# Kernel optimization log

Measured on AMD Instinct MI355X. Metric: run time of the kernel, lower is better.

## Reference

```python
import jax, jax.numpy as jnp
import numpy as np

N_EMBD = 1024
COND = 1024
N_HEAD = 16
B, N, NTOK = 4, 2048, 2048


def setup_inputs() -> dict:
    key = jax.random.key(0)
    ks = jax.random.split(key, 10)
    s = 0.02
    return {
        "x": jax.random.normal(ks[0], (B, N, N_EMBD), jnp.float32),
        "encoder_output": jax.random.normal(ks[1], (B, NTOK, COND), jnp.float32),
        "Wq": jax.random.normal(ks[2], (N_EMBD, N_EMBD), jnp.float32) * s,
        "bq": jnp.zeros((N_EMBD,), jnp.float32),
        "Wk": jax.random.normal(ks[3], (N_EMBD, COND), jnp.float32) * s,
        "bk": jnp.zeros((N_EMBD,), jnp.float32),
        "Wv": jax.random.normal(ks[4], (N_EMBD, COND), jnp.float32) * s,
        "bv": jnp.zeros((N_EMBD,), jnp.float32),
        "Wp": jax.random.normal(ks[5], (N_EMBD, N_EMBD), jnp.float32) * s,
        "bp": jnp.zeros((N_EMBD,), jnp.float32),
    }


def reference(x, encoder_output, Wq, bq, Wk, bk, Wv, bv, Wp, bp):
    Bx, Nx, C = x.shape
    H = N_HEAD
    D = C // H
    # projections (torch Linear: y = x @ W^T + b)
    q = (x @ Wq.T + bq).reshape(Bx, Nx, H, D)               # b n h d
    k = (encoder_output @ Wk.T + bk).reshape(Bx, -1, H, D)  # b t h d
    v = (encoder_output @ Wv.T + bv).reshape(Bx, -1, H, D)
    scale = 1.0 / jnp.sqrt(jnp.asarray(D, x.dtype))
    att = jnp.einsum("bnhd,bthd->bhnt", q, k) * scale
    att = jax.nn.softmax(att, axis=-1)
    y = jnp.einsum("bhnt,bthd->bnhd", att, v).reshape(Bx, Nx, C)
    y = y @ Wp.T + bp  # dropout is identity at inference (p effectively 0)
    return y
```

## Files before the change

kernel.cpp:

```cpp
#include <hip/hip_runtime.h>

typedef short bf16x8 __attribute__((ext_vector_type(8)));
typedef float f32x4 __attribute__((ext_vector_type(4)));
typedef unsigned int u32x2 __attribute__((ext_vector_type(2)));
typedef unsigned int u32x4 __attribute__((ext_vector_type(4)));

#define AS1 __attribute__((address_space(1)))
#define AS3 __attribute__((address_space(3)))

__device__ __forceinline__ void gld16(void* lds, const void* g) {
  __builtin_amdgcn_global_load_lds((const AS1 unsigned int*)g,
                                   (AS3 unsigned int*)lds, 16, 0, 0);
}

__device__ __forceinline__ unsigned short f2bf(float f) {
  union { float f; unsigned int u; } c; c.f = f;
  return (unsigned short)((c.u + 0x7FFFu + ((c.u >> 16) & 1u)) >> 16);
}

__device__ __forceinline__ unsigned short cvt1(float x) {
  unsigned int r;
  asm("v_cvt_pk_bf16_f32 %0, %1, %1" : "=v"(r) : "v"(x));
  return (unsigned short)r;
}

__device__ __forceinline__ unsigned int cvtpk(float lo, float hi) {
  unsigned int r;
  asm("v_cvt_pk_bf16_f32 %0, %1, %2" : "=v"(r) : "v"(lo), "v"(hi));
  return r;
}

__device__ __forceinline__ float bf2f(unsigned short u) {
  union { unsigned int u; float f; } c; c.u = ((unsigned int)u) << 16;
  return c.f;
}

__device__ __forceinline__ float fmax3(float a, float b, float c) {
  return fmaxf(fmaxf(a, b), c);
}

__global__ void cvt_kernel(const float4* __restrict__ in0,
                           const float4* __restrict__ in1,
                           ushort4* __restrict__ out0,
                           ushort4* __restrict__ out1, int n4) {
  const float4* in = blockIdx.y ? in1 : in0;
  ushort4* out = blockIdx.y ? out1 : out0;
  int i = blockIdx.x * blockDim.x + threadIdx.x;
  int stride = gridDim.x * blockDim.x;
  for (; i < n4; i += stride) {
    float4 v = in[i];
    ushort4 o;
    o.x = f2bf(v.x); o.y = f2bf(v.y); o.z = f2bf(v.z); o.w = f2bf(v.w);
    out[i] = o;
  }
}

__global__ void cvtw_kernel(const float4* w0, const float4* w1,
                            const float4* w2, const float4* w3,
                            ushort4* o0, ushort4* o1, ushort4* o2, ushort4* o3,
                            int n4) {
  const float4* in; ushort4* out;
  switch (blockIdx.y) {
    case 0: in = w0; out = o0; break;
    case 1: in = w1; out = o1; break;
    case 2: in = w2; out = o2; break;
    default: in = w3; out = o3; break;
  }
  int i = blockIdx.x * blockDim.x + threadIdx.x;
  int stride = gridDim.x * blockDim.x;
  for (; i < n4; i += stride) {
    float4 v = in[i];
    ushort4 o;
    o.x = f2bf(v.x); o.y = f2bf(v.y); o.z = f2bf(v.z); o.w = f2bf(v.w);
    out[i] = o;
  }
}

__global__ __launch_bounds__(256) void gemm_qkv_kernel(
    const unsigned short* __restrict__ Xb,
    const unsigned short* __restrict__ Eb,
    const unsigned short* __restrict__ Wqb,
    const unsigned short* __restrict__ Wkb,
    const unsigned short* __restrict__ Wvb,
    const float* __restrict__ bq,
    const float* __restrict__ bk,
    const float* __restrict__ bv,
    unsigned short* __restrict__ Qw,
    unsigned short* __restrict__ Kw,
    unsigned short* __restrict__ VTw,
    float qscale)
{
  __shared__ alignas(16) unsigned short As[2][4 * 128 * 8];
  __shared__ alignas(16) unsigned short Bs[2][4 * 128 * 8];

  const int bid = blockIdx.x;
  const int o = (bid & 7) * 192 + (bid >> 3);
  const int xx = o % 24;
  const int yy = o / 24;
  const int sec = xx >> 3;
  const int nx = xx & 7;

  const unsigned short* A = (sec == 0) ? Xb : Eb;
  const unsigned short* W = (sec == 0) ? Wqb : (sec == 1) ? Wkb : Wvb;
  const float* bias = (sec == 0) ? bq : (sec == 1) ? bk : bv;

  const int K = 1024, N = 1024;
  const int tid = threadIdx.x;
  const int lane = tid & 63;
  const int w = tid >> 6;
  const int wr = (w >> 1) * 64;
  const int wc = (w & 1) * 64;
  const int lrow = lane & 15;
  const int lk = lane >> 4;
  const long m0 = (long)yy * 128;
  const long n0 = (long)nx * 128;

  f32x4 acc[4][4] = {};

  const int c0 = tid, c1 = tid + 256;
  const unsigned short* Ag0 = A + (m0 + (c0 & 127)) * (long)K + (c0 >> 7) * 8;
  const unsigned short* Ag1 = A + (m0 + (c1 & 127)) * (long)K + (c1 >> 7) * 8;
  const unsigned short* Wg0 = W + (n0 + (c0 & 127)) * (long)K + (c0 >> 7) * 8;
  const unsigned short* Wg1 = W + (n0 + (c1 & 127)) * (long)K + (c1 >> 7) * 8;

  const int arow = wr + lrow;
  const int brow = wc + lrow;
  const int nt = K >> 5;

  gld16(As[0] + c0 * 8, Ag0);
  gld16(As[0] + c1 * 8, Ag1);
  gld16(Bs[0] + c0 * 8, Wg0);
  gld16(Bs[0] + c1 * 8, Wg1);

  int cur = 0;
  for (int t = 0; t < nt; ++t) {
    __syncthreads();
    if (t + 1 < nt) {
      const int kt = (t + 1) * 32;
      gld16(As[cur ^ 1] + c0 * 8, Ag0 + kt);
      gld16(As[cur ^ 1] + c1 * 8, Ag1 + kt);
      gld16(Bs[cur ^ 1] + c0 * 8, Wg0 + kt);
      gld16(Bs[cur ^ 1] + c1 * 8, Wg1 + kt);
    }
    const unsigned short* as = As[cur];
    const unsigned short* bs = Bs[cur];
    bf16x8 af[4], bfr[4];
#pragma unroll
    for (int i = 0; i < 4; ++i)
      af[i] = *(const bf16x8*)(as + (lk * 128 + arow + i * 16) * 8);
#pragma unroll
    for (int j = 0; j < 4; ++j)
      bfr[j] = *(const bf16x8*)(bs + (lk * 128 + brow + j * 16) * 8);
    if (sec != 2) {
#pragma unroll
      for (int i = 0; i < 4; ++i)
#pragma unroll
        for (int j = 0; j < 4; ++j)
          acc[i][j] = __builtin_amdgcn_mfma_f32_16x16x32_bf16(af[i], bfr[j], acc[i][j], 0, 0, 0);
    } else {
#pragma unroll
      for (int i = 0; i < 4; ++i)
#pragma unroll
        for (int j = 0; j < 4; ++j)
          acc[i][j] = __builtin_amdgcn_mfma_f32_16x16x32_bf16(bfr[i], af[j], acc[i][j], 0, 0, 0);
    }
    cur ^= 1;
  }

  if (sec != 2) {
    unsigned short* out = (sec == 0) ? Qw : Kw;
    const float scale = (sec == 0) ? qscale : 1.0f;
#pragma unroll
    for (int j = 0; j < 4; ++j) {
      const long col = n0 + wc + j * 16 + lrow;
      const float bv_ = bias[col];
#pragma unroll
      for (int i = 0; i < 4; ++i)
#pragma unroll
        for (int r = 0; r < 4; ++r) {
          const long row = m0 + wr + i * 16 + lk * 4 + r;
          out[row * (long)N + col] = cvt1((acc[i][j][r] + bv_) * scale);
        }
    }
  } else {
#pragma unroll
    for (int i = 0; i < 4; ++i)
#pragma unroll
      for (int r = 0; r < 4; ++r) {
        const long feat = n0 + wc + i * 16 + lk * 4 + r;
        const float bv_ = bias[feat];
#pragma unroll
        for (int j = 0; j < 4; ++j) {
          const long col = m0 + wr + j * 16 + lrow;
          VTw[feat * 8192 + col] = cvt1(acc[i][j][r] + bv_);
        }
      }
  }
}

__global__ __launch_bounds__(256) void gemm_p_kernel(
    const unsigned short* __restrict__ A,
    const unsigned short* __restrict__ W,
    const float* __restrict__ bias,
    float* __restrict__ outF)
{
  __shared__ alignas(16) unsigned short As[2][4 * 128 * 8];
  __shared__ alignas(16) unsigned short Bs[2][4 * 128 * 8];

  const int bid = blockIdx.x;
  const int o = (bid & 7) * 64 + (bid >> 3);
  const int nx = o & 7;
  const int yy = o >> 3;

  const int K = 1024, N = 1024;
  const int tid = threadIdx.x;
  const int lane = tid & 63;
  const int w = tid >> 6;
  const int wr = (w >> 1) * 64;
  const int wc = (w & 1) * 64;
  const int lrow = lane & 15;
  const int lk = lane >> 4;
  const long m0 = (long)yy * 128;
  const long n0 = (long)nx * 128;

  f32x4 acc[4][4] = {};

  const int c0 = tid, c1 = tid + 256;
  const unsigned short* Ag0 = A + (m0 + (c0 & 127)) * (long)K + (c0 >> 7) * 8;
  const unsigned short* Ag1 = A + (m0 + (c1 & 127)) * (long)K + (c1 >> 7) * 8;
  const unsigned short* Wg0 = W + (n0 + (c0 & 127)) * (long)K + (c0 >> 7) * 8;
  const unsigned short* Wg1 = W + (n0 + (c1 & 127)) * (long)K + (c1 >> 7) * 8;

  const int arow = wr + lrow;
  const int brow = wc + lrow;
  const int nt = K >> 5;

  gld16(As[0] + c0 * 8, Ag0);
  gld16(As[0] + c1 * 8, Ag1);
  gld16(Bs[0] + c0 * 8, Wg0);
  gld16(Bs[0] + c1 * 8, Wg1);

  int cur = 0;
  for (int t = 0; t < nt; ++t) {
    __syncthreads();
    if (t + 1 < nt) {
      const int kt = (t + 1) * 32;
      gld16(As[cur ^ 1] + c0 * 8, Ag0 + kt);
      gld16(As[cur ^ 1] + c1 * 8, Ag1 + kt);
      gld16(Bs[cur ^ 1] + c0 * 8, Wg0 + kt);
      gld16(Bs[cur ^ 1] + c1 * 8, Wg1 + kt);
    }
    const unsigned short* as = As[cur];
    const unsigned short* bs = Bs[cur];
    bf16x8 af[4], bfr[4];
#pragma unroll
    for (int i = 0; i < 4; ++i)
      af[i] = *(const bf16x8*)(as + (lk * 128 + arow + i * 16) * 8);
#pragma unroll
    for (int j = 0; j < 4; ++j)
      bfr[j] = *(const bf16x8*)(bs + (lk * 128 + brow + j * 16) * 8);
#pragma unroll
    for (int i = 0; i < 4; ++i)
#pragma unroll
      for (int j = 0; j < 4; ++j)
        acc[i][j] = __builtin_amdgcn_mfma_f32_16x16x32_bf16(af[i], bfr[j], acc[i][j], 0, 0, 0);
    cur ^= 1;
  }

#pragma unroll
  for (int j = 0; j < 4; ++j) {
    const long col = n0 + wc + j * 16 + lrow;
    const float bv_ = bias[col];
#pragma unroll
    for (int i = 0; i < 4; ++i)
#pragma unroll
      for (int r = 0; r < 4; ++r) {
        const long row = m0 + wr + i * 16 + lk * 4 + r;
        outF[row * (long)N + col] = acc[i][j][r] + bv_;
      }
  }
}

__global__ __launch_bounds__(256) void attn_kernel(
    const unsigned short* __restrict__ Q,
    const unsigned short* __restrict__ K,
    const unsigned short* __restrict__ VT,
    unsigned short* __restrict__ Op,
    float2* __restrict__ Lm)
{
  __shared__ alignas(16) unsigned short Ks[2][8 * 64 * 8];
  __shared__ alignas(16) unsigned short Vt[2][64 * 64];
  __shared__ alignas(16) unsigned short Ps[128 * 72];

  const int tid = threadIdx.x;
  const int lane = tid & 63;
  const int w = tid >> 6;
  const int lrow = lane & 15;
  const int lk = lane >> 4;

  const int id = blockIdx.x;
  const int r8 = id & 7;
  const int qt = (id >> 3) & 15;
  const int sp = (id >> 7) & 1;
  const int s = id >> 8;
  const int bh = r8 + 8 * s;
  const int h = bh & 15, b = bh >> 4;
  const long C = 1024, T = 2048, NQ = 2048;
  const int kt0 = sp * 1024;
  const int ktEnd = kt0 + 1024;

  const unsigned short* Qg = Q + ((long)b * NQ + qt * 128) * C + h * 64;
  const unsigned short* Kg0 = K + (long)b * T * C + h * 64;
  const unsigned short* Vg0 = VT + (long)(h * 64) * 8192 + b * 2048;

  {
    int c = tid;
    gld16(Ks[0] + c * 8, Kg0 + (long)(kt0 + (c & 63)) * C + (c >> 6) * 8);
    c = tid + 256;
    gld16(Ks[0] + c * 8, Kg0 + (long)(kt0 + (c & 63)) * C + (c >> 6) * 8);
    c = tid;
    gld16(Vt[0] + c * 8, Vg0 + (long)(c >> 3) * 8192 + kt0 + (((c & 7) ^ ((c >> 3) & 7)) * 8));
    c = tid + 256;
    gld16(Vt[0] + c * 8, Vg0 + (long)(c >> 3) * 8192 + kt0 + (((c & 7) ^ ((c >> 3) & 7)) * 8));
  }
  bf16x8 qf[2][2];
#pragma unroll
  for (int f = 0; f < 2; ++f)
#pragma unroll
    for (int kk = 0; kk < 2; ++kk)
      qf[f][kk] = *(const bf16x8*)(Qg + (long)(f * 64 + w * 16 + lrow) * C + (kk * 4 + lk) * 8);

  bf16x8 ones;
#pragma unroll
  for (int e = 0; e < 8; ++e) ones[e] = (short)0x3F80;

  __syncthreads();

  f32x4 oA[4] = {}, oB[4] = {};
  f32x4 olA = {}, olB = {};
  float mrA = 0.f, mrB = 0.f;
  int cur = 0;

  const int qrow0 = w * 16 + lrow;

  for (int kt = kt0; kt < ktEnd; kt += 64) {
    const bool more = (kt + 64 < ktEnd);
    if (more) {
      int c = tid;
      gld16(Ks[cur ^ 1] + c * 8, Kg0 + (long)(kt + 64 + (c & 63)) * C + (c >> 6) * 8);
      gld16(Vt[cur ^ 1] + c * 8,
            Vg0 + (long)(c >> 3) * 8192 + kt + 64 + (((c & 7) ^ ((c >> 3) & 7)) * 8));
      c = tid + 256;
      gld16(Ks[cur ^ 1] + c * 8, Kg0 + (long)(kt + 64 + (c & 63)) * C + (c >> 6) * 8);
      gld16(Vt[cur ^ 1] + c * 8,
            Vg0 + (long)(c >> 3) * 8192 + kt + 64 + (((c & 7) ^ ((c >> 3) & 7)) * 8));
    }

    f32x4 sA[4], sB[4];
#pragma unroll
    for (int j = 0; j < 4; ++j)
#pragma unroll
      for (int r = 0; r < 4; ++r) { sA[j][r] = -mrA; sB[j][r] = -mrB; }

    __builtin_amdgcn_s_setprio(1);
#pragma unroll
    for (int kk = 0; kk < 2; ++kk) {
#pragma unroll
      for (int j = 0; j < 4; ++j) {
        bf16x8 kf = *(const bf16x8*)(Ks[cur] + ((kk * 4 + lk) * 64 + j * 16 + lrow) * 8);
        sA[j] = __builtin_amdgcn_mfma_f32_16x16x32_bf16(kf, qf[0][kk], sA[j], 0, 0, 0);
        sB[j] = __builtin_amdgcn_mfma_f32_16x16x32_bf16(kf, qf[1][kk], sB[j], 0, 0, 0);
      }
    }
    __builtin_amdgcn_s_setprio(0);

    float pmA, pmB;
    {
      float a0 = fmax3(sA[0][0], sA[0][1], sA[0][2]);
      float a1 = fmax3(sA[0][3], sA[1][0], sA[1][1]);
      float a2 = fmax3(sA[1][2], sA[1][3], sA[2][0]);
      float a3 = fmax3(sA[2][1], sA[2][2], sA[2][3]);
      float a4 = fmax3(sA[3][0], sA[3][1], sA[3][2]);
      pmA = fmax3(fmax3(a0, a1, a2), fmax3(a3, a4, sA[3][3]),
                  __shfl_xor(fmax3(a0, a1, a2), 16));
      float t = fmax3(fmax3(a0, a1, a2), a3, fmax3(a4, sA[3][3], sA[3][3]));
      t = fmaxf(t, __shfl_xor(t, 16));
      t = fmaxf(t, __shfl_xor(t, 32));
      pmA = t;
      float b0 = fmax3(sB[0][0], sB[0][1], sB[0][2]);
      float b1 = fmax3(sB[0][3], sB[1][0], sB[1][1]);
      float b2 = fmax3(sB[1][2], sB[1][3], sB[2][0]);
      float b3 = fmax3(sB[2][1], sB[2][2], sB[2][3]);
      float b4 = fmax3(sB[3][0], sB[3][1], sB[3][2]);
      float u = fmax3(fmax3(b0, b1, b2), b3, fmax3(b4, sB[3][3], sB[3][3]));
      u = fmaxf(u, __shfl_xor(u, 16));
      u = fmaxf(u, __shfl_xor(u, 32));
      pmB = u;
    }
    if (__any(fmaxf(pmA, pmB) > 8.0f)) {
      const float dmA = fmaxf(pmA, 0.f);
      const float alA = __builtin_amdgcn_exp2f(-dmA);
      mrA += dmA; olA *= alA;
      const float dmB = fmaxf(pmB, 0.f);
      const float alB = __builtin_amdgcn_exp2f(-dmB);
      mrB += dmB; olB *= alB;
#pragma unroll
      for (int j = 0; j < 4; ++j) {
        oA[j] *= alA;
        oB[j] *= alB;
#pragma unroll
        for (int r = 0; r < 4; ++r) { sA[j][r] -= dmA; sB[j][r] -= dmB; }
      }
    }
#pragma unroll
    for (int j = 0; j < 4; ++j) {
      float p0 = __builtin_amdgcn_exp2f(sA[j][0]);
      float p1 = __builtin_amdgcn_exp2f(sA[j][1]);
      float p2 = __builtin_amdgcn_exp2f(sA[j][2]);
      float p3 = __builtin_amdgcn_exp2f(sA[j][3]);
      u32x2 pk;
      pk.x = cvtpk(p0, p1);
      pk.y = cvtpk(p2, p3);
      *(u32x2*)(Ps + qrow0 * 72 + j * 16 + lk * 4) = pk;
    }
#pragma unroll
    for (int j = 0; j < 4; ++j) {
      float p0 = __builtin_amdgcn_exp2f(sB[j][0]);
      float p1 = __builtin_amdgcn_exp2f(sB[j][1]);
      float p2 = __builtin_amdgcn_exp2f(sB[j][2]);
      float p3 = __builtin_amdgcn_exp2f(sB[j][3]);
      u32x2 pk;
      pk.x = cvtpk(p0, p1);
      pk.y = cvtpk(p2, p3);
      *(u32x2*)(Ps + (64 + qrow0) * 72 + j * 16 + lk * 4) = pk;
    }

    const unsigned short* vt = Vt[cur];
    __builtin_amdgcn_s_setprio(1);
#pragma unroll
    for (int kk = 0; kk < 2; ++kk) {
      bf16x8 pa0 = *(const bf16x8*)(Ps + qrow0 * 72 + kk * 32 + lk * 8);
      bf16x8 pa1 = *(const bf16x8*)(Ps + (64 + qrow0) * 72 + kk * 32 + lk * 8);
      olA = __builtin_amdgcn_mfma_f32_16x16x32_bf16(ones, pa0, olA, 0, 0, 0);
      olB = __builtin_amdgcn_mfma_f32_16x16x32_bf16(ones, pa1, olB, 0, 0, 0);
#pragma unroll
      for (int j = 0; j < 4; ++j) {
        const int d = j * 16 + lrow;
        bf16x8 vb = *(const bf16x8*)(vt + d * 64 + ((((kk * 4 + lk) ^ (d & 7)) & 7) << 3));
        oA[j] = __builtin_amdgcn_mfma_f32_16x16x32_bf16(vb, pa0, oA[j], 0, 0, 0);
        oB[j] = __builtin_amdgcn_mfma_f32_16x16x32_bf16(vb, pa1, oB[j], 0, 0, 0);
      }
    }
    __builtin_amdgcn_s_setprio(0);

    cur ^= 1;
    __syncthreads();
  }

  const long base = ((long)sp * 64 + bh) * 2048;
  const long qlA = base + qt * 128 + qrow0;
  const long qlB = qlA + 64;
#pragma unroll
  for (int j = 0; j < 4; ++j) {
    u32x2 pk;
    pk.x = cvtpk(oA[j][0], oA[j][1]);
    pk.y = cvtpk(oA[j][2], oA[j][3]);
    *(u32x2*)(Op + qlA * 64 + j * 16 + lk * 4) = pk;
    pk.x = cvtpk(oB[j][0], oB[j][1]);
    pk.y = cvtpk(oB[j][2], oB[j][3]);
    *(u32x2*)(Op + qlB * 64 + j * 16 + lk * 4) = pk;
  }
  if (lk == 0) {
    Lm[qlA] = make_float2(olA[0], mrA);
    Lm[qlB] = make_float2(olB[0], mrB);
  }
}

__global__ __launch_bounds__(256) void attn_combine_kernel(
    const unsigned short* __restrict__ Op,
    const float2* __restrict__ Lm,
    unsigned short* __restrict__ Y)
{
  const int t = blockIdx.x * 256 + threadIdx.x;
  const int d0 = t & 7;
  const int ql = (t >> 3) & 2047;
  const int bh = t >> 14;
  const long row = (long)bh * 2048 + ql;
  const float2 lm0 = Lm[row];
  const float2 lm1 = Lm[131072 + row];
  const float m = fmaxf(lm0.y, lm1.y);
  const float w0 = __builtin_amdgcn_exp2f(lm0.y - m);
  const float w1 = __builtin_amdgcn_exp2f(lm1.y - m);
  const float dn = 1.f / (lm0.x * w0 + lm1.x * w1);
  const float c0 = w0 * dn, c1 = w1 * dn;
  bf16x8 o0 = *(const bf16x8*)(Op + row * 64 + d0 * 8);
  bf16x8 o1 = *(const bf16x8*)(Op + (131072L + row) * 64 + d0 * 8);
  u32x4 pk;
  float v0, v1;
  v0 = bf2f((unsigned short)o0[0]) * c0 + bf2f((unsigned short)o1[0]) * c1;
  v1 = bf2f((unsigned short)o0[1]) * c0 + bf2f((unsigned short)o1[1]) * c1;
  pk.x = cvtpk(v0, v1);
  v0 = bf2f((unsigned short)o0[2]) * c0 + bf2f((unsigned short)o1[2]) * c1;
  v1 = bf2f((unsigned short)o0[3]) * c0 + bf2f((unsigned short)o1[3]) * c1;
  pk.y = cvtpk(v0, v1);
  v0 = bf2f((unsigned short)o0[4]) * c0 + bf2f((unsigned short)o1[4]) * c1;
  v1 = bf2f((unsigned short)o0[5]) * c0 + bf2f((unsigned short)o1[5]) * c1;
  pk.z = cvtpk(v0, v1);
  v0 = bf2f((unsigned short)o0[6]) * c0 + bf2f((unsigned short)o1[6]) * c1;
  v1 = bf2f((unsigned short)o0[7]) * c0 + bf2f((unsigned short)o1[7]) * c1;
  pk.w = cvtpk(v0, v1);
  const int b = bh >> 4, h = bh & 15;
  *(u32x4*)(Y + ((long)b * 2048 + ql) * 1024 + h * 64 + d0 * 8) = pk;
}

extern "C" void kernel_launch(void* const* d_in, const int* in_sizes, int n_in,
                              void* d_out, int out_size, void* d_ws, size_t ws_size,
                              hipStream_t stream) {
  (void)in_sizes; (void)n_in; (void)out_size; (void)ws_size;
  const float* x   = (const float*)d_in[0];
  const float* enc = (const float*)d_in[1];
  const float* Wq  = (const float*)d_in[2];
  const float* bq  = (const float*)d_in[3];
  const float* Wk  = (const float*)d_in[4];
  const float* bk  = (const float*)d_in[5];
  const float* Wv  = (const float*)d_in[6];
  const float* bv  = (const float*)d_in[7];
  const float* Wp  = (const float*)d_in[8];
  const float* bp  = (const float*)d_in[9];

  const long M = 4L * 2048;
  const long C = 1024;

  char* ws = (char*)d_ws;
  size_t off = 0;
  auto alloc = [&](size_t bytes) {
    char* p = ws + off;
    off += (bytes + 255) & ~(size_t)255;
    return p;
  };
  unsigned short* Xb  = (unsigned short*)alloc(M * C * 2);
  unsigned short* Eb  = (unsigned short*)alloc(M * C * 2);
  unsigned short* Wqb = (unsigned short*)alloc(C * C * 2);
  unsigned short* Wkb = (unsigned short*)alloc(C * C * 2);
  unsigned short* Wvb = (unsigned short*)alloc(C * C * 2);
  unsigned short* Wpb = (unsigned short*)alloc(C * C * 2);
  unsigned short* Qw  = (unsigned short*)alloc(M * C * 2);
  unsigned short* Kw  = (unsigned short*)alloc(M * C * 2);
  unsigned short* VTw = (unsigned short*)alloc(M * C * 2);
  unsigned short* Yb  = (unsigned short*)alloc(M * C * 2);
  float2* Lm = (float2*)alloc(2L * 64 * 2048 * sizeof(float2));

  unsigned short* Op = Xb;

  {
    int n4 = (int)(M * C / 4);
    int blocks = (n4 + 255) / 256; if (blocks > 2048) blocks = 2048;
    cvt_kernel<<<dim3(blocks, 2), 256, 0, stream>>>(
        (const float4*)x, (const float4*)enc, (ushort4*)Xb, (ushort4*)Eb, n4);
    int w4 = (int)(C * C / 4);
    cvtw_kernel<<<dim3(1024, 4), 256, 0, stream>>>(
        (const float4*)Wq, (const float4*)Wk, (const float4*)Wv, (const float4*)Wp,
        (ushort4*)Wqb, (ushort4*)Wkb, (ushort4*)Wvb, (ushort4*)Wpb, w4);
  }

  const float qscale = 0.125f * 1.44269504088896f;
  gemm_qkv_kernel<<<1536, 256, 0, stream>>>(
      Xb, Eb, Wqb, Wkb, Wvb, bq, bk, bv, Qw, Kw, VTw, qscale);

  attn_kernel<<<2048, 256, 0, stream>>>(Qw, Kw, VTw, Op, Lm);
  attn_combine_kernel<<<4096, 256, 0, stream>>>(Op, Lm, Yb);

  gemm_p_kernel<<<512, 256, 0, stream>>>(Yb, Wpb, bp, (float*)d_out);
}
```

Measured before the change: 285.1 us.

## Replace double-buffered LDS DMA prefetch with register-staged single-buffer K/V loads

```diff
diff --git a/kernel.cpp b/kernel.cpp
--- a/kernel.cpp
+++ b/kernel.cpp
@@ -288,8 +288,8 @@
     unsigned short* __restrict__ Op,
     float2* __restrict__ Lm)
 {
-  __shared__ alignas(16) unsigned short Ks[2][8 * 64 * 8];
-  __shared__ alignas(16) unsigned short Vt[2][64 * 64];
+  __shared__ alignas(16) unsigned short Ks[8 * 64 * 8];
+  __shared__ alignas(16) unsigned short Vt[64 * 64];
   __shared__ alignas(16) unsigned short Ps[128 * 72];
 
   const int tid = threadIdx.x;
@@ -313,15 +313,21 @@
   const unsigned short* Kg0 = K + (long)b * T * C + h * 64;
   const unsigned short* Vg0 = VT + (long)(h * 64) * 8192 + b * 2048;
 
+  const int c0 = tid, c1 = tid + 256;
+  const unsigned short* Kg_c0 = Kg0 + (long)(c0 & 63) * C + (c0 >> 6) * 8;
+  const unsigned short* Kg_c1 = Kg0 + (long)(c1 & 63) * C + (c1 >> 6) * 8;
+  const unsigned short* Vg_c0 = Vg0 + (long)(c0 >> 3) * 8192 + (((c0 & 7) ^ ((c0 >> 3) & 7)) * 8);
+  const unsigned short* Vg_c1 = Vg0 + (long)(c1 >> 3) * 8192 + (((c1 & 7) ^ ((c1 >> 3) & 7)) * 8);
+
   {
-    int c = tid;
-    gld16(Ks[0] + c * 8, Kg0 + (long)(kt0 + (c & 63)) * C + (c >> 6) * 8);
-    c = tid + 256;
-    gld16(Ks[0] + c * 8, Kg0 + (long)(kt0 + (c & 63)) * C + (c >> 6) * 8);
-    c = tid;
-    gld16(Vt[0] + c * 8, Vg0 + (long)(c >> 3) * 8192 + kt0 + (((c & 7) ^ ((c >> 3) & 7)) * 8));
-    c = tid + 256;
-    gld16(Vt[0] + c * 8, Vg0 + (long)(c >> 3) * 8192 + kt0 + (((c & 7) ^ ((c >> 3) & 7)) * 8));
+    bf16x8 k0 = *(const bf16x8*)(Kg_c0 + (long)kt0 * C);
+    bf16x8 k1 = *(const bf16x8*)(Kg_c1 + (long)kt0 * C);
+    bf16x8 v0 = *(const bf16x8*)(Vg_c0 + kt0);
+    bf16x8 v1 = *(const bf16x8*)(Vg_c1 + kt0);
+    *(bf16x8*)(Ks + c0 * 8) = k0;
+    *(bf16x8*)(Ks + c1 * 8) = k1;
+    *(bf16x8*)(Vt + c0 * 8) = v0;
+    *(bf16x8*)(Vt + c1 * 8) = v1;
   }
   bf16x8 qf[2][2];
 #pragma unroll
@@ -339,21 +345,17 @@
   f32x4 oA[4] = {}, oB[4] = {};
   f32x4 olA = {}, olB = {};
   float mrA = 0.f, mrB = 0.f;
-  int cur = 0;
 
   const int qrow0 = w * 16 + lrow;
 
   for (int kt = kt0; kt < ktEnd; kt += 64) {
     const bool more = (kt + 64 < ktEnd);
+    bf16x8 nk0, nk1, nv0, nv1;
     if (more) {
-      int c = tid;
-      gld16(Ks[cur ^ 1] + c * 8, Kg0 + (long)(kt + 64 + (c & 63)) * C + (c >> 6) * 8);
-      gld16(Vt[cur ^ 1] + c * 8,
-            Vg0 + (long)(c >> 3) * 8192 + kt + 64 + (((c & 7) ^ ((c >> 3) & 7)) * 8));
-      c = tid + 256;
-      gld16(Ks[cur ^ 1] + c * 8, Kg0 + (long)(kt + 64 + (c & 63)) * C + (c >> 6) * 8);
-      gld16(Vt[cur ^ 1] + c * 8,
-            Vg0 + (long)(c >> 3) * 8192 + kt + 64 + (((c & 7) ^ ((c >> 3) & 7)) * 8));
+      nk0 = *(const bf16x8*)(Kg_c0 + (long)(kt + 64) * C);
+      nk1 = *(const bf16x8*)(Kg_c1 + (long)(kt + 64) * C);
+      nv0 = *(const bf16x8*)(Vg_c0 + kt + 64);
+      nv1 = *(const bf16x8*)(Vg_c1 + kt + 64);
     }
 
     f32x4 sA[4], sB[4];
@@ -367,7 +369,7 @@
     for (int kk = 0; kk < 2; ++kk) {
 #pragma unroll
       for (int j = 0; j < 4; ++j) {
-        bf16x8 kf = *(const bf16x8*)(Ks[cur] + ((kk * 4 + lk) * 64 + j * 16 + lrow) * 8);
+        bf16x8 kf = *(const bf16x8*)(Ks + ((kk * 4 + lk) * 64 + j * 16 + lrow) * 8);
         sA[j] = __builtin_amdgcn_mfma_f32_16x16x32_bf16(kf, qf[0][kk], sA[j], 0, 0, 0);
         sB[j] = __builtin_amdgcn_mfma_f32_16x16x32_bf16(kf, qf[1][kk], sB[j], 0, 0, 0);
       }
@@ -381,9 +383,7 @@
       float a2 = fmax3(sA[1][2], sA[1][3], sA[2][0]);
       float a3 = fmax3(sA[2][1], sA[2][2], sA[2][3]);
       float a4 = fmax3(sA[3][0], sA[3][1], sA[3][2]);
-      pmA = fmax3(fmax3(a0, a1, a2), fmax3(a3, a4, sA[3][3]),
-                  __shfl_xor(fmax3(a0, a1, a2), 16));
-      float t = fmax3(fmax3(a0, a1, a2), a3, fmax3(a4, sA[3][3], sA[3][3]));
+      float t = fmax3(fmax3(a0, a1, a2), a3, fmaxf(a4, sA[3][3]));
       t = fmaxf(t, __shfl_xor(t, 16));
       t = fmaxf(t, __shfl_xor(t, 32));
       pmA = t;
@@ -392,7 +392,7 @@
       float b2 = fmax3(sB[1][2], sB[1][3], sB[2][0]);
       float b3 = fmax3(sB[2][1], sB[2][2], sB[2][3]);
       float b4 = fmax3(sB[3][0], sB[3][1], sB[3][2]);
-      float u = fmax3(fmax3(b0, b1, b2), b3, fmax3(b4, sB[3][3], sB[3][3]));
+      float u = fmax3(fmax3(b0, b1, b2), b3, fmaxf(b4, sB[3][3]));
       u = fmaxf(u, __shfl_xor(u, 16));
       u = fmaxf(u, __shfl_xor(u, 32));
       pmB = u;
@@ -435,7 +435,6 @@
       *(u32x2*)(Ps + (64 + qrow0) * 72 + j * 16 + lk * 4) = pk;
     }
 
-    const unsigned short* vt = Vt[cur];
     __builtin_amdgcn_s_setprio(1);
 #pragma unroll
     for (int kk = 0; kk < 2; ++kk) {
@@ -446,14 +445,20 @@
 #pragma unroll
       for (int j = 0; j < 4; ++j) {
         const int d = j * 16 + lrow;
-        bf16x8 vb = *(const bf16x8*)(vt + d * 64 + ((((kk * 4 + lk) ^ (d & 7)) & 7) << 3));
+        bf16x8 vb = *(const bf16x8*)(Vt + d * 64 + ((((kk * 4 + lk) ^ (d & 7)) & 7) << 3));
         oA[j] = __builtin_amdgcn_mfma_f32_16x16x32_bf16(vb, pa0, oA[j], 0, 0, 0);
         oB[j] = __builtin_amdgcn_mfma_f32_16x16x32_bf16(vb, pa1, oB[j], 0, 0, 0);
       }
     }
     __builtin_amdgcn_s_setprio(0);
 
-    cur ^= 1;
+    __syncthreads();
+    if (more) {
+      *(bf16x8*)(Ks + c0 * 8) = nk0;
+      *(bf16x8*)(Ks + c1 * 8) = nk1;
+      *(bf16x8*)(Vt + c0 * 8) = nv0;
+      *(bf16x8*)(Vt + c1 * 8) = nv1;
+    }
     __syncthreads();
   }
 
```

After: 305.5 us. +7.1%, slower.
